# Performance work log

Measured on AMD Instinct MI355X. Metric: run time of the kernel, lower is better.

Reference implementation:

```python
import jax, jax.numpy as jnp
import numpy as np

N, K, D = 65536, 4096, 256
COMMITMENT_COST = 0.25


def setup_inputs() -> dict:
    key = jax.random.key(0)
    k1, k2 = jax.random.split(key)
    z_flat = jax.random.normal(k1, (N, D), dtype=jnp.float32)
    # init_method='normal': std=0.02
    codebook = jax.random.normal(k2, (K, D), dtype=jnp.float32) * 0.02
    return {"z_flat": z_flat, "codebook": codebook}


def reference(z_flat, codebook):
    # distances[n,k] = ||z_n||^2 + ||e_k||^2 - 2 z_n . e_k   (squared L2)
    z_sq = jnp.sum(z_flat ** 2, axis=1, keepdims=True)            # [N,1]
    e_sq = jnp.sum(codebook ** 2, axis=1)                          # [K]
    distances = z_sq + e_sq - 2.0 * jnp.matmul(z_flat, codebook.T)  # [N,K]
    indices = jnp.argmin(distances, axis=1)                        # [N] int
    quantized = codebook[indices]                                  # [N,D]

    e_latent_loss = jnp.mean((jax.lax.stop_gradient(quantized) - z_flat) ** 2)
    q_latent_loss = jnp.mean((quantized - jax.lax.stop_gradient(z_flat)) ** 2)
    loss = q_latent_loss + COMMITMENT_COST * e_latent_loss

    # straight-through estimator
    quantized_st = z_flat + jax.lax.stop_gradient(quantized - z_flat)
    return loss, quantized_st, indices
```

## Files before the change

kernel.cpp:

```cpp
#include <hip/hip_runtime.h>
#include <float.h>

typedef __attribute__((ext_vector_type(8))) short short8;
typedef __attribute__((ext_vector_type(16))) float f32x16;
typedef unsigned short u16;

#define N_ROWS 65536
#define K_CB   4096
#define D_DIM  256
#define TAU    1.0e-3f
#define RR     8

#define RB 128
#define KB 128
#define DB 32

#define WS_COUNTER 0
#define WS_ESQ     16
#define WS_IDX     (WS_ESQ + K_CB*4)
#define WS_FLAG    (WS_IDX + N_ROWS*4)
#define WS_PART    (WS_FLAG + N_ROWS*4)
#define NUM_OUT_BLOCKS ((N_ROWS*(D_DIM/4))/256)
#define WS_EH      (WS_PART + NUM_OUT_BLOCKS*8)
#define WS_EL      (WS_EH + K_CB*D_DIM*2)
#define WS_NEEDED  (WS_EL + (size_t)K_CB*D_DIM*2)

__device__ __forceinline__ u16 f2bf(float x) {
  unsigned int u = __float_as_uint(x);
  unsigned int r = (u + 0x7fffu + ((u >> 16) & 1u)) >> 16;
  return (u16)r;
}
__device__ __forceinline__ float bf2f(u16 b) {
  return __uint_as_float((unsigned int)b << 16);
}

__device__ __forceinline__ float np_sum128_sq(const float* p) {
#pragma clang fp contract(off)
  float r0 = p[0]*p[0], r1 = p[1]*p[1], r2 = p[2]*p[2], r3 = p[3]*p[3];
  float r4 = p[4]*p[4], r5 = p[5]*p[5], r6 = p[6]*p[6], r7 = p[7]*p[7];
  for (int i = 8; i < 128; i += 8) {
    r0 += p[i+0]*p[i+0]; r1 += p[i+1]*p[i+1];
    r2 += p[i+2]*p[i+2]; r3 += p[i+3]*p[i+3];
    r4 += p[i+4]*p[i+4]; r5 += p[i+5]*p[i+5];
    r6 += p[i+6]*p[i+6]; r7 += p[i+7]*p[i+7];
  }
  return ((r0+r1)+(r2+r3))+((r4+r5)+(r6+r7));
}
__device__ __forceinline__ float np_sumsq256(const float* p) {
#pragma clang fp contract(off)
  float a = np_sum128_sq(p);
  float b = np_sum128_sq(p + 128);
  return a + b;
}

__global__ __launch_bounds__(256) void esq_np_kernel(const float* __restrict__ cb,
                                                     float* __restrict__ esq) {
  const int k = blockIdx.x * 256 + threadIdx.x;
  esq[k] = np_sumsq256(cb + (size_t)k * D_DIM);
}

__global__ __launch_bounds__(256) void esplit_perm_kernel(const float* __restrict__ cb,
                                                          u16* __restrict__ ehp,
                                                          u16* __restrict__ elp) {
  const int g  = blockIdx.x * 256 + threadIdx.x;
  const int k  = g >> 5;
  const int d8 = g & 31;
  const int kc = k >> 5, c = k & 31;
  const float* src = cb + (size_t)k * D_DIM + d8 * 8;
  float4 f0 = *(const float4*)src;
  float4 f1 = *(const float4*)(src + 4);
  float f[8] = {f0.x, f0.y, f0.z, f0.w, f1.x, f1.y, f1.z, f1.w};
  short8 h, lo;
  #pragma unroll
  for (int j = 0; j < 8; ++j) {
    u16 hb = f2bf(f[j]);
    h[j]  = (short)hb;
    lo[j] = (short)f2bf(f[j] - bf2f(hb));
  }
  const size_t off = (size_t)kc * 8192 + (size_t)d8 * 256 + (size_t)c * 8;
  *(short8*)(ehp + off) = h;
  *(short8*)(elp + off) = lo;
}

__global__ __launch_bounds__(256, 2) void mfma_argmin32_kernel(
    const float* __restrict__ z, const u16* __restrict__ ehp,
    const u16* __restrict__ elp, const float* __restrict__ esq,
    int* __restrict__ idx_out, int* __restrict__ flag,
    unsigned int* __restrict__ counter) {
  __shared__ u16 smem[2 * 16384];
  const int t   = threadIdx.x;
  const int w   = t >> 6;
  const int l   = t & 63;
  const int col = l & 31;
  const int hi  = l >> 5;
  const int row = blockIdx.x * 128 + w * 32 + col;

  short8 ah[16], al[16];
  {
    const float* zr = z + (size_t)row * D_DIM + hi * 8;
    #pragma unroll
    for (int s = 0; s < 16; ++s) {
      float4 f0 = *(const float4*)(zr + s * 16);
      float4 f1 = *(const float4*)(zr + s * 16 + 4);
      float f[8] = {f0.x, f0.y, f0.z, f0.w, f1.x, f1.y, f1.z, f1.w};
      short8 h, lo;
      #pragma unroll
      for (int j = 0; j < 8; ++j) {
        u16 hb = f2bf(f[j]);
        h[j]  = (short)hb;
        lo[j] = (short)f2bf(f[j] - bf2f(hb));
      }
      ah[s] = h; al[s] = lo;
    }
  }

  float m1[16], m2[16]; int ic[16];
  #pragma unroll
  for (int r = 0; r < 16; ++r) { m1[r] = FLT_MAX; m2[r] = FLT_MAX; ic[r] = 0; }

  uint4 stg[8];
  {
    #pragma unroll
    for (int q = 0; q < 4; ++q) {
      stg[q]     = *(const uint4*)(ehp + q * 2048 + t * 8);
      stg[4 + q] = *(const uint4*)(elp + q * 2048 + t * 8);
    }
    char* b = (char*)smem;
    #pragma unroll
    for (int q = 0; q < 4; ++q) {
      *(uint4*)(b + q * 4096 + t * 16)         = stg[q];
      *(uint4*)(b + 16384 + q * 4096 + t * 16) = stg[4 + q];
    }
  }
  __syncthreads();

  const int boff = hi * 512 + col * 16;
  for (int kc = 0; kc < 128; ++kc) {
    const int cur = kc & 1;
    if (kc + 1 < 128) {
      const u16* s0 = ehp + (size_t)(kc + 1) * 8192;
      const u16* s1 = elp + (size_t)(kc + 1) * 8192;
      #pragma unroll
      for (int q = 0; q < 4; ++q) {
        stg[q]     = *(const uint4*)(s0 + q * 2048 + t * 8);
        stg[4 + q] = *(const uint4*)(s1 + q * 2048 + t * 8);
      }
    }
    const float ev = esq[kc * 32 + col];
    const char* bb = (const char*)smem + cur * 32768;
    f32x16 acc = {};
    #pragma unroll
    for (int s = 0; s < 16; ++s) {
      short8 bh = *(const short8*)(bb + s * 1024 + boff);
      short8 bl = *(const short8*)(bb + 16384 + s * 1024 + boff);
      acc = __builtin_amdgcn_mfma_f32_32x32x16_bf16(ah[s], bh, acc, 0, 0, 0);
      acc = __builtin_amdgcn_mfma_f32_32x32x16_bf16(al[s], bh, acc, 0, 0, 0);
      acc = __builtin_amdgcn_mfma_f32_32x32x16_bf16(ah[s], bl, acc, 0, 0, 0);
    }
    #pragma unroll
    for (int r = 0; r < 16; ++r) {
      float sc = fmaf(-2.0f, acc[r], ev);
      bool lt = sc < m1[r];
      ic[r] = lt ? kc : ic[r];
      m2[r] = fminf(m2[r], fmaxf(m1[r], sc));
      m1[r] = fminf(m1[r], sc);
    }
    if (kc + 1 < 128) {
      char* b = (char*)smem + (cur ^ 1) * 32768;
      #pragma unroll
      for (int q = 0; q < 4; ++q) {
        *(uint4*)(b + q * 4096 + t * 16)         = stg[q];
        *(uint4*)(b + 16384 + q * 4096 + t * 16) = stg[4 + q];
      }
    }
    __syncthreads();
  }

  #pragma unroll
  for (int r = 0; r < 16; ++r) {
    float a1 = m1[r], a2 = m2[r];
    int cd = ic[r] * 32 + col;
    #pragma unroll
    for (int off = 1; off < 32; off <<= 1) {
      float b1 = __shfl_xor(a1, off);
      float b2 = __shfl_xor(a2, off);
      int   bc = __shfl_xor(cd, off);
      bool take = (b1 < a1) || (b1 == a1 && bc < cd);
      float nm2 = take ? fminf(a1, b2) : fminf(a2, b1);
      if (take) { a1 = b1; cd = bc; }
      a2 = nm2;
    }
    if (col == 0) {
      const int orow = blockIdx.x * 128 + w * 32 + (r & 3) + 8 * (r >> 2) + 4 * hi;
      idx_out[orow] = cd;
      if (a2 - a1 < TAU) {
        unsigned int p = atomicAdd(counter, 1u);
        flag[p] = orow;
      }
    }
  }
}

__global__ __launch_bounds__(256, 2) void argmin_kernel(
    const float4* __restrict__ z4, const float4* __restrict__ cb4,
    const float* __restrict__ esq, int* __restrict__ idx_out,
    int* __restrict__ flag, unsigned int* __restrict__ counter) {
  __shared__ float zt[DB][RB];
  __shared__ float et[DB][KB];
  const int t  = threadIdx.x;
  const int tr = t >> 4;
  const int tc = t & 15;
  const int row0 = blockIdx.x * RB;

  float min1[8], min2[8]; int idx1[8];
  #pragma unroll
  for (int i = 0; i < 8; ++i) { min1[i] = FLT_MAX; min2[i] = FLT_MAX; idx1[i] = 0; }

  for (int kc = 0; kc < K_CB / KB; ++kc) {
    const int k0 = kc * KB;
    float acc[8][8];
    #pragma unroll
    for (int i = 0; i < 8; ++i)
      #pragma unroll
      for (int j = 0; j < 8; ++j) acc[i][j] = 0.0f;

    float esqv[8];
    #pragma unroll
    for (int j = 0; j < 8; ++j) esqv[j] = esq[k0 + tc*8 + j];

    for (int dt = 0; dt < D_DIM / DB; ++dt) {
      __syncthreads();
      #pragma unroll
      for (int m = 0; m < 4; ++m) {
        int u  = t + 256*m;
        int dq = u & 7;
        int r  = u >> 3;
        float4 v = z4[(size_t)(row0 + r)*(D_DIM/4) + dt*8 + dq];
        zt[dq*4+0][r] = v.x; zt[dq*4+1][r] = v.y; zt[dq*4+2][r] = v.z; zt[dq*4+3][r] = v.w;
        float4 wv = cb4[(size_t)(k0 + r)*(D_DIM/4) + dt*8 + dq];
        et[dq*4+0][r] = wv.x; et[dq*4+1][r] = wv.y; et[dq*4+2][r] = wv.z; et[dq*4+3][r] = wv.w;
      }
      __syncthreads();

      #pragma unroll 8
      for (int d = 0; d < DB; ++d) {
        float4 za = *(const float4*)&zt[d][tr*8];
        float4 zb = *(const float4*)&zt[d][tr*8+4];
        float4 ea = *(const float4*)&et[d][tc*8];
        float4 eb = *(const float4*)&et[d][tc*8+4];
        float zr[8] = {za.x, za.y, za.z, za.w, zb.x, zb.y, zb.z, zb.w};
        float ev[8] = {ea.x, ea.y, ea.z, ea.w, eb.x, eb.y, eb.z, eb.w};
        #pragma unroll
        for (int i = 0; i < 8; ++i)
          #pragma unroll
          for (int j = 0; j < 8; ++j)
            acc[i][j] += zr[i] * ev[j];
      }
    }

    #pragma unroll
    for (int j = 0; j < 8; ++j) {
      const int k = k0 + tc*8 + j;
      #pragma unroll
      for (int i = 0; i < 8; ++i) {
        float s = esqv[j] - 2.0f * acc[i][j];
        if (s < min1[i]) { min2[i] = min1[i]; min1[i] = s; idx1[i] = k; }
        else if (s < min2[i]) { min2[i] = s; }
      }
    }
  }

  #pragma unroll
  for (int i = 0; i < 8; ++i) {
    float m1 = min1[i], m2 = min2[i]; int id = idx1[i];
    #pragma unroll
    for (int off = 1; off < 16; off <<= 1) {
      float om1 = __shfl_xor(m1, off);
      float om2 = __shfl_xor(m2, off);
      int   oid = __shfl_xor(id, off);
      bool take = (om1 < m1) || (om1 == m1 && oid < id);
      float nm2 = take ? fminf(m1, om2) : fminf(m2, om1);
      if (take) { m1 = om1; id = oid; }
      m2 = nm2;
    }
    if (tc == 0) {
      int row = row0 + tr*8 + i;
      idx_out[row] = id;
      if (m2 - m1 < TAU) {
        unsigned int p = atomicAdd(counter, 1u);
        flag[p] = row;
      }
    }
  }
}

__global__ __launch_bounds__(256) void refine_np_kernel(
    const float* __restrict__ z, const float* __restrict__ cb,
    const float* __restrict__ esq, int* __restrict__ idx_out,
    const int* __restrict__ flag, const unsigned int* __restrict__ counter) {
  __shared__ float zrow[RR][D_DIM];
  __shared__ float zsq[RR];
  __shared__ float rbest[256];
  __shared__ int   rbidx[256];
  const int t = threadIdx.x;
  const unsigned int cnt = *counter;
  const unsigned int ngroups = (cnt + RR - 1) / RR;

  for (unsigned int g = blockIdx.x; g < ngroups; g += gridDim.x) {
    __syncthreads();
    const int nr = (int)min((unsigned int)RR, cnt - g*RR);
    #pragma unroll
    for (int r = 0; r < RR; ++r) {
      int fi = (int)(g*RR) + ((r < nr) ? r : 0);
      int row = flag[fi];
      zrow[r][t] = z[(size_t)row * D_DIM + t];
    }
    __syncthreads();
    if (t < RR) zsq[t] = np_sumsq256(&zrow[t][0]);
    __syncthreads();

    float best[RR]; int bidx[RR];
    #pragma unroll
    for (int r = 0; r < RR; ++r) { best[r] = FLT_MAX; bidx[r] = 0x7fffffff; }

    for (int m = 0; m < K_CB / 256; ++m) {
      const int k = m*256 + t;
      const float4* e4 = (const float4*)(cb + (size_t)k * D_DIM);
      float acc[RR];
      #pragma unroll
      for (int r = 0; r < RR; ++r) acc[r] = 0.0f;
      for (int dq = 0; dq < D_DIM/4; ++dq) {
        float4 ev = e4[dq];
        #pragma unroll
        for (int r = 0; r < RR; ++r) {
          acc[r] = __fmaf_rn(zrow[r][dq*4+0], ev.x, acc[r]);
          acc[r] = __fmaf_rn(zrow[r][dq*4+1], ev.y, acc[r]);
          acc[r] = __fmaf_rn(zrow[r][dq*4+2], ev.z, acc[r]);
          acc[r] = __fmaf_rn(zrow[r][dq*4+3], ev.w, acc[r]);
        }
      }
      const float ek = esq[k];
      #pragma unroll
      for (int r = 0; r < RR; ++r) {
#pragma clang fp contract(off)
        float u1 = zsq[r] + ek;
        float u2 = 2.0f * acc[r];
        float sc = u1 - u2;
        if (sc < best[r]) { best[r] = sc; bidx[r] = k; }
      }
    }

    for (int r = 0; r < RR; ++r) {
      __syncthreads();
      rbest[t] = best[r]; rbidx[t] = bidx[r];
      __syncthreads();
      for (int off = 128; off > 0; off >>= 1) {
        if (t < off) {
          float ob = rbest[t+off]; int oi = rbidx[t+off];
          if (ob < rbest[t] || (ob == rbest[t] && oi < rbidx[t])) {
            rbest[t] = ob; rbidx[t] = oi;
          }
        }
        __syncthreads();
      }
      if (t == 0 && r < nr) idx_out[flag[g*RR + r]] = rbidx[0];
    }
  }
}

__global__ __launch_bounds__(256) void output_kernel(
    const float4* __restrict__ z4, const float4* __restrict__ cb4,
    const int* __restrict__ idx_out, float* __restrict__ out,
    double* __restrict__ partials) {
  const int g  = blockIdx.x * 256 + threadIdx.x;
  const int n  = g >> 6;
  const int dq = g & 63;
  const int id = idx_out[n];
  float4 q  = cb4[(size_t)id * (D_DIM/4) + dq];
  float4 zv = z4[(size_t)n  * (D_DIM/4) + dq];
  float dx = q.x - zv.x, dy = q.y - zv.y, dz = q.z - zv.z, dw = q.w - zv.w;
  double psum = (double)dx*dx + (double)dy*dy + (double)dz*dz + (double)dw*dw;
  size_t base = 1 + (size_t)n * D_DIM + (size_t)dq * 4;
  out[base+0] = q.x; out[base+1] = q.y; out[base+2] = q.z; out[base+3] = q.w;
  if (dq == 0) out[1 + (size_t)N_ROWS*D_DIM + n] = (float)id;

  __shared__ double sred[256];
  sred[threadIdx.x] = psum;
  __syncthreads();
  for (int off = 128; off > 0; off >>= 1) {
    if (threadIdx.x < off) sred[threadIdx.x] += sred[threadIdx.x + off];
    __syncthreads();
  }
  if (threadIdx.x == 0) partials[blockIdx.x] = sred[0];
}

__global__ __launch_bounds__(256) void loss_kernel(const double* __restrict__ partials,
                                                   float* __restrict__ out) {
  const int t = threadIdx.x;
  double s = 0.0;
  for (int m = 0; m < NUM_OUT_BLOCKS/256; ++m) s += partials[t + 256*m];
  __shared__ double sred[256];
  sred[t] = s;
  __syncthreads();
  for (int off = 128; off > 0; off >>= 1) {
    if (t < off) sred[t] += sred[t + off];
    __syncthreads();
  }
  if (t == 0) out[0] = (float)(1.25 * sred[0] / ((double)N_ROWS * (double)D_DIM));
}

extern "C" void kernel_launch(void* const* d_in, const int* in_sizes, int n_in,
                              void* d_out, int out_size, void* d_ws, size_t ws_size,
                              hipStream_t stream) {
  const float* z  = (const float*)d_in[0];
  const float* cb = (const float*)d_in[1];
  float* out = (float*)d_out;
  char* ws = (char*)d_ws;

  unsigned int* counter = (unsigned int*)(ws + WS_COUNTER);
  float*  esq      = (float*) (ws + WS_ESQ);
  int*    idx      = (int*)   (ws + WS_IDX);
  int*    flag     = (int*)   (ws + WS_FLAG);
  double* partials = (double*)(ws + WS_PART);

  hipMemsetAsync(ws, 0, 16, stream);
  esq_np_kernel<<<K_CB/256, 256, 0, stream>>>(cb, esq);

  if (ws_size >= WS_NEEDED) {
    u16* ehp = (u16*)(ws + WS_EH);
    u16* elp = (u16*)(ws + WS_EL);
    esplit_perm_kernel<<<(K_CB*(D_DIM/8))/256, 256, 0, stream>>>(cb, ehp, elp);
    mfma_argmin32_kernel<<<N_ROWS/128, 256, 0, stream>>>(z, ehp, elp, esq,
                                                         idx, flag, counter);
  } else {
    argmin_kernel<<<N_ROWS/RB, 256, 0, stream>>>((const float4*)z, (const float4*)cb,
                                                 esq, idx, flag, counter);
  }

  refine_np_kernel<<<256, 256, 0, stream>>>(z, cb, esq, idx, flag, counter);
  output_kernel<<<NUM_OUT_BLOCKS, 256, 0, stream>>>((const float4*)z, (const float4*)cb,
                                                    idx, out, partials);
  loss_kernel<<<1, 256, 0, stream>>>(partials, out);
}
```

Before: 570.6 us.

## Split MFMA chain into three accumulators and interleave staged codebook prefetch

The main argmin kernel now keeps three independent MFMA accumulators (hi*hi, lo*hi, hi*lo) instead of one serial chain, removing the dependency stalls between back-to-back MFMAs on the same accumulator. The next codebook tile is staged in two halves (high part, then low part), with the stores and loads placed between the two halves of the MFMA loop, which halves the staging registers and overlaps global loads with compute. The cost is two extra 16-float accumulators, and the summation order changes slightly, which could shift near-tie distances that the refine pass has to catch. The score helper and the memset cast are cosmetic refactors.

```diff
diff --git a/kernel.cpp b/kernel.cpp
--- a/kernel.cpp
+++ b/kernel.cpp
@@ -32,6 +32,12 @@
 }
 __device__ __forceinline__ float bf2f(u16 b) {
   return __uint_as_float((unsigned int)b << 16);
+}
+__device__ __forceinline__ float np_score(float zsq, float ek, float dot) {
+#pragma clang fp contract(off)
+  float t1 = zsq + ek;
+  float t2 = 2.0f * dot;
+  return t1 - t2;
 }
 
 __device__ __forceinline__ float np_sum128_sq(const float* p) {
@@ -118,60 +124,79 @@
   #pragma unroll
   for (int r = 0; r < 16; ++r) { m1[r] = FLT_MAX; m2[r] = FLT_MAX; ic[r] = 0; }
 
-  uint4 stg[8];
+  uint4 stg[4];
   {
     #pragma unroll
-    for (int q = 0; q < 4; ++q) {
-      stg[q]     = *(const uint4*)(ehp + q * 2048 + t * 8);
-      stg[4 + q] = *(const uint4*)(elp + q * 2048 + t * 8);
-    }
-    char* b = (char*)smem;
-    #pragma unroll
-    for (int q = 0; q < 4; ++q) {
-      *(uint4*)(b + q * 4096 + t * 16)         = stg[q];
-      *(uint4*)(b + 16384 + q * 4096 + t * 16) = stg[4 + q];
-    }
+    for (int q = 0; q < 4; ++q)
+      stg[q] = *(const uint4*)((const char*)ehp + q * 4096 + t * 16);
+    #pragma unroll
+    for (int q = 0; q < 4; ++q)
+      *(uint4*)((char*)smem + q * 4096 + t * 16) = stg[q];
+    #pragma unroll
+    for (int q = 0; q < 4; ++q)
+      stg[q] = *(const uint4*)((const char*)elp + q * 4096 + t * 16);
+    #pragma unroll
+    for (int q = 0; q < 4; ++q)
+      *(uint4*)((char*)smem + 16384 + q * 4096 + t * 16) = stg[q];
   }
   __syncthreads();
 
   const int boff = hi * 512 + col * 16;
   for (int kc = 0; kc < 128; ++kc) {
     const int cur = kc & 1;
-    if (kc + 1 < 128) {
-      const u16* s0 = ehp + (size_t)(kc + 1) * 8192;
-      const u16* s1 = elp + (size_t)(kc + 1) * 8192;
-      #pragma unroll
-      for (int q = 0; q < 4; ++q) {
-        stg[q]     = *(const uint4*)(s0 + q * 2048 + t * 8);
-        stg[4 + q] = *(const uint4*)(s1 + q * 2048 + t * 8);
-      }
-    }
-    const float ev = esq[kc * 32 + col];
     const char* bb = (const char*)smem + cur * 32768;
-    f32x16 acc = {};
-    #pragma unroll
-    for (int s = 0; s < 16; ++s) {
+    char* wb = (char*)smem + (cur ^ 1) * 32768;
+    const bool hn = (kc + 1 < 128);
+
+    if (hn) {
+      #pragma unroll
+      for (int q = 0; q < 4; ++q)
+        stg[q] = *(const uint4*)((const char*)ehp + (size_t)(kc + 1) * 16384 + q * 4096 + t * 16);
+    }
+
+    f32x16 ahh = {}, alh = {}, ahl = {};
+    #pragma unroll
+    for (int s = 0; s < 8; ++s) {
       short8 bh = *(const short8*)(bb + s * 1024 + boff);
       short8 bl = *(const short8*)(bb + 16384 + s * 1024 + boff);
-      acc = __builtin_amdgcn_mfma_f32_32x32x16_bf16(ah[s], bh, acc, 0, 0, 0);
-      acc = __builtin_amdgcn_mfma_f32_32x32x16_bf16(al[s], bh, acc, 0, 0, 0);
-      acc = __builtin_amdgcn_mfma_f32_32x32x16_bf16(ah[s], bl, acc, 0, 0, 0);
-    }
+      ahh = __builtin_amdgcn_mfma_f32_32x32x16_bf16(ah[s], bh, ahh, 0, 0, 0);
+      alh = __builtin_amdgcn_mfma_f32_32x32x16_bf16(al[s], bh, alh, 0, 0, 0);
+      ahl = __builtin_amdgcn_mfma_f32_32x32x16_bf16(ah[s], bl, ahl, 0, 0, 0);
+    }
+
+    if (hn) {
+      #pragma unroll
+      for (int q = 0; q < 4; ++q)
+        *(uint4*)(wb + q * 4096 + t * 16) = stg[q];
+      #pragma unroll
+      for (int q = 0; q < 4; ++q)
+        stg[q] = *(const uint4*)((const char*)elp + (size_t)(kc + 1) * 16384 + q * 4096 + t * 16);
+    }
+
+    #pragma unroll
+    for (int s = 8; s < 16; ++s) {
+      short8 bh = *(const short8*)(bb + s * 1024 + boff);
+      short8 bl = *(const short8*)(bb + 16384 + s * 1024 + boff);
+      ahh = __builtin_amdgcn_mfma_f32_32x32x16_bf16(ah[s], bh, ahh, 0, 0, 0);
+      alh = __builtin_amdgcn_mfma_f32_32x32x16_bf16(al[s], bh, alh, 0, 0, 0);
+      ahl = __builtin_amdgcn_mfma_f32_32x32x16_bf16(ah[s], bl, ahl, 0, 0, 0);
+    }
+
+    const float ev = esq[kc * 32 + col];
     #pragma unroll
     for (int r = 0; r < 16; ++r) {
-      float sc = fmaf(-2.0f, acc[r], ev);
+      float sum = (ahh[r] + alh[r]) + ahl[r];
+      float sc = fmaf(-2.0f, sum, ev);
       bool lt = sc < m1[r];
       ic[r] = lt ? kc : ic[r];
       m2[r] = fminf(m2[r], fmaxf(m1[r], sc));
       m1[r] = fminf(m1[r], sc);
     }
-    if (kc + 1 < 128) {
-      char* b = (char*)smem + (cur ^ 1) * 32768;
-      #pragma unroll
-      for (int q = 0; q < 4; ++q) {
-        *(uint4*)(b + q * 4096 + t * 16)         = stg[q];
-        *(uint4*)(b + 16384 + q * 4096 + t * 16) = stg[4 + q];
-      }
+
+    if (hn) {
+      #pragma unroll
+      for (int q = 0; q < 4; ++q)
+        *(uint4*)(wb + 16384 + q * 4096 + t * 16) = stg[q];
     }
     __syncthreads();
   }
@@ -342,10 +367,7 @@
       const float ek = esq[k];
       #pragma unroll
       for (int r = 0; r < RR; ++r) {
-#pragma clang fp contract(off)
-        float u1 = zsq[r] + ek;
-        float u2 = 2.0f * acc[r];
-        float sc = u1 - u2;
+        float sc = np_score(zsq[r], ek, acc[r]);
         if (sc < best[r]) { best[r] = sc; bidx[r] = k; }
       }
     }
@@ -423,7 +445,7 @@
   int*    flag     = (int*)   (ws + WS_FLAG);
   double* partials = (double*)(ws + WS_PART);
 
-  hipMemsetAsync(ws, 0, 16, stream);
+  (void)hipMemsetAsync(ws, 0, 16, stream);
   esq_np_kernel<<<K_CB/256, 256, 0, stream>>>(cb, esq);
 
   if (ws_size >= WS_NEEDED) {
```

New measurement: 695.7 us. +21.9%, slower.

## Stage codebook tiles via direct global-to-LDS loads and split MFMA accumulators

Applied to the files above, without the earlier changes.

Replaces the register-staged prefetch (global load into registers, then store to LDS) with global_load_lds builtins that write the next codebook tile straight into shared memory. This frees the staging registers and removes the LDS store instructions. The single MFMA accumulator chain is also split into four rotating accumulators, summed before the score, to break the serial dependency between consecutive MFMAs. The risk is correctness of the async LDS writes, since only __syncthreads guards them with no explicit vmcnt wait, and the changed summation order perturbs the near-tie scores.

```diff
diff --git a/kernel.cpp b/kernel.cpp
--- a/kernel.cpp
+++ b/kernel.cpp
@@ -32,6 +32,12 @@
 }
 __device__ __forceinline__ float bf2f(u16 b) {
   return __uint_as_float((unsigned int)b << 16);
+}
+__device__ __forceinline__ float np_score(float zsq, float ek, float dot) {
+#pragma clang fp contract(off)
+  float t1 = zsq + ek;
+  float t2 = 2.0f * dot;
+  return t1 - t2;
 }
 
 __device__ __forceinline__ float np_sum128_sq(const float* p) {
@@ -94,6 +100,7 @@
   const int col = l & 31;
   const int hi  = l >> 5;
   const int row = blockIdx.x * 128 + w * 32 + col;
+  const int wbase = w * 1024;
 
   short8 ah[16], al[16];
   {
@@ -118,63 +125,63 @@
   #pragma unroll
   for (int r = 0; r < 16; ++r) { m1[r] = FLT_MAX; m2[r] = FLT_MAX; ic[r] = 0; }
 
-  uint4 stg[8];
-  {
-    #pragma unroll
-    for (int q = 0; q < 4; ++q) {
-      stg[q]     = *(const uint4*)(ehp + q * 2048 + t * 8);
-      stg[4 + q] = *(const uint4*)(elp + q * 2048 + t * 8);
-    }
-    char* b = (char*)smem;
-    #pragma unroll
-    for (int q = 0; q < 4; ++q) {
-      *(uint4*)(b + q * 4096 + t * 16)         = stg[q];
-      *(uint4*)(b + 16384 + q * 4096 + t * 16) = stg[4 + q];
-    }
-  }
+  #define STAGE(KCN, BUF) do {                                                  \
+    char* lb = (char*)smem + (BUF) * 32768;                                     \
+    const char* gh = (const char*)ehp + (size_t)(KCN) * 16384;                  \
+    const char* gl = (const char*)elp + (size_t)(KCN) * 16384;                  \
+    _Pragma("unroll")                                                           \
+    for (int q = 0; q < 4; ++q) {                                               \
+      __builtin_amdgcn_global_load_lds(                                         \
+        (const __attribute__((address_space(1))) void*)(gh + q*4096 + t*16),    \
+        (__attribute__((address_space(3))) void*)(lb + q*4096 + wbase),         \
+        16, 0, 0);                                                              \
+      __builtin_amdgcn_global_load_lds(                                         \
+        (const __attribute__((address_space(1))) void*)(gl + q*4096 + t*16),    \
+        (__attribute__((address_space(3))) void*)(lb + 16384 + q*4096 + wbase), \
+        16, 0, 0);                                                              \
+    }                                                                           \
+  } while (0)
+
+  STAGE(0, 0);
   __syncthreads();
 
   const int boff = hi * 512 + col * 16;
   for (int kc = 0; kc < 128; ++kc) {
     const int cur = kc & 1;
-    if (kc + 1 < 128) {
-      const u16* s0 = ehp + (size_t)(kc + 1) * 8192;
-      const u16* s1 = elp + (size_t)(kc + 1) * 8192;
-      #pragma unroll
-      for (int q = 0; q < 4; ++q) {
-        stg[q]     = *(const uint4*)(s0 + q * 2048 + t * 8);
-        stg[4 + q] = *(const uint4*)(s1 + q * 2048 + t * 8);
-      }
-    }
+    if (kc + 1 < 128) STAGE(kc + 1, cur ^ 1);
+    const char* bb = (const char*)smem + cur * 32768;
+
+    f32x16 c0 = {}, c1 = {}, c2 = {}, c3 = {};
+    #define MFMA3(S, A0, A1, A2) do {                                           \
+      short8 bh = *(const short8*)(bb + (S) * 1024 + boff);                     \
+      short8 bl = *(const short8*)(bb + 16384 + (S) * 1024 + boff);             \
+      A0 = __builtin_amdgcn_mfma_f32_32x32x16_bf16(ah[S], bh, A0, 0, 0, 0);     \
+      A1 = __builtin_amdgcn_mfma_f32_32x32x16_bf16(al[S], bh, A1, 0, 0, 0);     \
+      A2 = __builtin_amdgcn_mfma_f32_32x32x16_bf16(ah[S], bl, A2, 0, 0, 0);     \
+    } while (0)
+    MFMA3(0,  c0, c1, c2);  MFMA3(1,  c3, c0, c1);
+    MFMA3(2,  c2, c3, c0);  MFMA3(3,  c1, c2, c3);
+    MFMA3(4,  c0, c1, c2);  MFMA3(5,  c3, c0, c1);
+    MFMA3(6,  c2, c3, c0);  MFMA3(7,  c1, c2, c3);
+    MFMA3(8,  c0, c1, c2);  MFMA3(9,  c3, c0, c1);
+    MFMA3(10, c2, c3, c0);  MFMA3(11, c1, c2, c3);
+    MFMA3(12, c0, c1, c2);  MFMA3(13, c3, c0, c1);
+    MFMA3(14, c2, c3, c0);  MFMA3(15, c1, c2, c3);
+    #undef MFMA3
+
     const float ev = esq[kc * 32 + col];
-    const char* bb = (const char*)smem + cur * 32768;
-    f32x16 acc = {};
-    #pragma unroll
-    for (int s = 0; s < 16; ++s) {
-      short8 bh = *(const short8*)(bb + s * 1024 + boff);
-      short8 bl = *(const short8*)(bb + 16384 + s * 1024 + boff);
-      acc = __builtin_amdgcn_mfma_f32_32x32x16_bf16(ah[s], bh, acc, 0, 0, 0);
-      acc = __builtin_amdgcn_mfma_f32_32x32x16_bf16(al[s], bh, acc, 0, 0, 0);
-      acc = __builtin_amdgcn_mfma_f32_32x32x16_bf16(ah[s], bl, acc, 0, 0, 0);
-    }
     #pragma unroll
     for (int r = 0; r < 16; ++r) {
-      float sc = fmaf(-2.0f, acc[r], ev);
+      float sum = (c0[r] + c1[r]) + (c2[r] + c3[r]);
+      float sc = fmaf(-2.0f, sum, ev);
       bool lt = sc < m1[r];
       ic[r] = lt ? kc : ic[r];
       m2[r] = fminf(m2[r], fmaxf(m1[r], sc));
       m1[r] = fminf(m1[r], sc);
     }
-    if (kc + 1 < 128) {
-      char* b = (char*)smem + (cur ^ 1) * 32768;
-      #pragma unroll
-      for (int q = 0; q < 4; ++q) {
-        *(uint4*)(b + q * 4096 + t * 16)         = stg[q];
-        *(uint4*)(b + 16384 + q * 4096 + t * 16) = stg[4 + q];
-      }
-    }
-    __syncthreads();
-  }
+    __syncthreads();
+  }
+  #undef STAGE
 
   #pragma unroll
   for (int r = 0; r < 16; ++r) {
@@ -342,10 +349,7 @@
       const float ek = esq[k];
       #pragma unroll
       for (int r = 0; r < RR; ++r) {
-#pragma clang fp contract(off)
-        float u1 = zsq[r] + ek;
-        float u2 = 2.0f * acc[r];
-        float sc = u1 - u2;
+        float sc = np_score(zsq[r], ek, acc[r]);
         if (sc < best[r]) { best[r] = sc; bidx[r] = k; }
       }
     }
@@ -423,7 +427,7 @@
   int*    flag     = (int*)   (ws + WS_FLAG);
   double* partials = (double*)(ws + WS_PART);
 
-  hipMemsetAsync(ws, 0, 16, stream);
+  (void)hipMemsetAsync(ws, 0, 16, stream);
   esq_np_kernel<<<K_CB/256, 256, 0, stream>>>(cb, esq);
 
   if (ws_size >= WS_NEEDED) {
```

New measurement: 599.7 us. 1.05x slower.
